# Kernel optimization log

Measured on AMD Instinct MI355X. Metric: run time of the kernel, lower is better.

The kernel has to match this reference:

```python
import jax, jax.numpy as jnp
import numpy as np

GRID_H, GRID_W, INPUT_DIM = 256, 256, 64
BATCH = 4096


def setup_inputs() -> dict:
    key = jax.random.key(0)
    k_in, k_w = jax.random.split(key)
    inputs = jax.random.uniform(k_in, (BATCH, INPUT_DIM), dtype=jnp.float32)
    # SOM weights initialized uniform[0,1) as in the original layer
    weights_map = jax.random.uniform(k_w, (GRID_H, GRID_W, INPUT_DIM), dtype=jnp.float32)
    return {"inputs": inputs, "weights_map": weights_map}


def reference(inputs, weights_map):
    """Inference forward of SOM2dLayer: find BMU coords + quantization error.

    inputs:      [B, D]
    weights_map: [H, W, D]
    returns (bmu_indices [B,2] int32, quantization_errors [B] float32)
    """
    H, W, D = weights_map.shape
    flat_w = weights_map.reshape(H * W, D)            # [N, D]
    x2 = jnp.sum(inputs * inputs, axis=1, keepdims=True)      # [B, 1]
    w2 = jnp.sum(flat_w * flat_w, axis=1)                     # [N]
    d2 = x2 - 2.0 * (inputs @ flat_w.T) + w2                  # [B, N]
    d2 = jnp.maximum(d2, 0.0)                                 # numerical floor
    bmu_flat = jnp.argmin(d2, axis=1)                         # [B]
    bmu_y = (bmu_flat // W).astype(jnp.int32)
    bmu_x = (bmu_flat % W).astype(jnp.int32)
    bmu_indices = jnp.stack([bmu_y, bmu_x], axis=1)           # [B, 2]
    min_d2 = jnp.take_along_axis(d2, bmu_flat[:, None], axis=1)[:, 0]
    quantization_errors = jnp.sqrt(min_d2)                    # [B]
    return bmu_indices, quantization_errors
```

## Files before the change

kernel.cpp:

```cpp
#include <hip/hip_runtime.h>
#include <math.h>


typedef short  bf16x8 __attribute__((ext_vector_type(8)));
typedef float  f32x4  __attribute__((ext_vector_type(4)));
typedef unsigned short u16;

constexpr int D     = 64;
constexpr int NW    = 65536;
constexpr int B     = 4096;
constexpr int NSUB  = 256;
constexpr int NFINE = NW / 16;
constexpr float MARG_HALF = 0.15f;

constexpr int STRIPS   = 32;
constexpr int STRIP_N  = NW / STRIPS;
constexpr int PANELS   = 8;
constexpr int ROWS_BLK = 128;

__device__ inline u16 bf16u(float f) {
    union { float f; unsigned u; } v; v.f = f;
    unsigned b = v.u;
    b += 0x7fffu + ((b >> 16) & 1u);
    return (u16)(b >> 16);
}

__device__ inline u16 bf16up(float f) {
    union { float f; unsigned u; } v; v.f = f;
    unsigned h = v.u >> 16;
    if ((v.u & 0xFFFFu) && !(v.u >> 31)) h += 1;
    return (u16)h;
}

__device__ __forceinline__ void gload_lds16(const void* g, void* l) {
    __builtin_amdgcn_global_load_lds(
        (const __attribute__((address_space(1))) unsigned int*)g,
        (__attribute__((address_space(3))) unsigned int*)l, 16, 0, 0);
}

__global__ __launch_bounds__(256) void k_prep(const float* __restrict__ w,
                                              const float* __restrict__ x,
                                              u16* __restrict__ whi,
                                              u16* __restrict__ xhi,
                                              float* __restrict__ w2c) {
    const int idx = blockIdx.x * 256 + threadIdx.x;
    if (idx < NW) {
        const float4* wr = reinterpret_cast<const float4*>(w + (size_t)idx * D);
        u16* orow = whi + (size_t)idx * D;
        float a0 = 0.f, a1 = 0.f, a2 = 0.f, a3 = 0.f;
#pragma unroll
        for (int h = 0; h < 8; ++h) {
            float4 v0 = wr[2 * h], v1 = wr[2 * h + 1];
            a0 = fmaf(v0.x, v0.x, a0); a1 = fmaf(v0.y, v0.y, a1);
            a2 = fmaf(v0.z, v0.z, a2); a3 = fmaf(v0.w, v0.w, a3);
            a0 = fmaf(v1.x, v1.x, a0); a1 = fmaf(v1.y, v1.y, a1);
            a2 = fmaf(v1.z, v1.z, a2); a3 = fmaf(v1.w, v1.w, a3);
            bf16x8 o = {(short)bf16u(v0.x), (short)bf16u(v0.y),
                        (short)bf16u(v0.z), (short)bf16u(v0.w),
                        (short)bf16u(v1.x), (short)bf16u(v1.y),
                        (short)bf16u(v1.z), (short)bf16u(v1.w)};
            *reinterpret_cast<bf16x8*>(orow + 8 * h) = o;
        }
        w2c[idx] = -0.5f * ((a0 + a1) + (a2 + a3));
    } else {
        const int r = idx - NW;
        const float4* xr = reinterpret_cast<const float4*>(x + (size_t)r * D);
        u16* orow = xhi + (size_t)r * D;
#pragma unroll
        for (int h = 0; h < 8; ++h) {
            float4 v0 = xr[2 * h], v1 = xr[2 * h + 1];
            bf16x8 o = {(short)bf16u(v0.x), (short)bf16u(v0.y),
                        (short)bf16u(v0.z), (short)bf16u(v0.w),
                        (short)bf16u(v1.x), (short)bf16u(v1.y),
                        (short)bf16u(v1.z), (short)bf16u(v1.w)};
            *reinterpret_cast<bf16x8*>(orow + 8 * h) = o;
        }
    }
}

template <int WRITE_FINE>
__global__ __launch_bounds__(256, 2) void k_screen0(
        const u16* __restrict__ whi, const u16* __restrict__ xhi,
        const float* __restrict__ w2c, float* __restrict__ pm,
        u16* __restrict__ pmf) {
    __shared__ __align__(16) char smem[32768];
    __shared__ __align__(16) float pmsh[512];
    const int bid   = blockIdx.x;
    const int strip = bid & 31;
    const int rbk   = bid >> 5;
    const int tid   = threadIdx.x;
    const int wv    = tid >> 6;
    const int lane  = tid & 63;
    const int col   = lane & 15;
    const int kg    = lane >> 4;
    const int row0  = rbk * ROWS_BLK;

    bf16x8 a[8][2];
#pragma unroll
    for (int rg = 0; rg < 8; ++rg)
#pragma unroll
        for (int h = 0; h < 2; ++h)
            a[rg][h] = *reinterpret_cast<const bf16x8*>(
                xhi + (size_t)(row0 + rg * 16 + col) * D + h * 32 + kg * 8);

    const char* wbase = (const char*)whi + (size_t)strip * STRIP_N * 128;
    unsigned soff[8];
#pragma unroll
    for (int i = 0; i < 8; ++i) {
        unsigned o = (unsigned)(i * 256 + tid) * 16;
        soff[i] = o ^ (((o >> 7) & 7u) << 4);
    }

    const unsigned msk = (unsigned)(col & 7) << 4;
    const float* w2s = w2c + strip * STRIP_N;

    float mx[8][4];
#pragma unroll
    for (int rg = 0; rg < 8; ++rg)
#pragma unroll
        for (int r = 0; r < 4; ++r) mx[rg][r] = -3.4e38f;

    for (int p = 0; p < PANELS; ++p) {
#pragma unroll
        for (int i = 0; i < 8; ++i)
            gload_lds16(wbase + (size_t)p * 32768 + soff[i],
                        &smem[i * 4096 + wv * 1024]);
        __syncthreads();

        const float* w2p = w2s + p * 256;
#pragma unroll
        for (int t = 0; t < 4; ++t) {
            const int nloc = wv * 64 + t * 16 + col;
            const unsigned u0 = (unsigned)nloc * 128 + kg * 16;
            const bf16x8 b0 = *reinterpret_cast<const bf16x8*>(smem + (u0 ^ msk));
            const bf16x8 b1 = *reinterpret_cast<const bf16x8*>(smem + ((u0 + 64) ^ msk));
            const float c = w2p[nloc];
            const f32x4 cq = {c, c, c, c};
#pragma unroll
            for (int rg = 0; rg < 8; ++rg) {
                f32x4 acc = __builtin_amdgcn_mfma_f32_16x16x32_bf16(a[rg][0], b0, cq, 0, 0, 0);
                acc = __builtin_amdgcn_mfma_f32_16x16x32_bf16(a[rg][1], b1, acc, 0, 0, 0);
                mx[rg][0] = fmaxf(mx[rg][0], acc[0]);
                mx[rg][1] = fmaxf(mx[rg][1], acc[1]);
                mx[rg][2] = fmaxf(mx[rg][2], acc[2]);
                mx[rg][3] = fmaxf(mx[rg][3], acc[3]);
            }
        }

        if ((p & 3) == 3) {
            const int s0 = strip * 8 + (p >> 2) * 4;
            const int s  = s0 + wv;

            __syncthreads();

            if (WRITE_FINE) {
                u16* st = reinterpret_cast<u16*>(smem);
#pragma unroll
                for (int rg = 0; rg < 8; ++rg)
#pragma unroll
                    for (int r = 0; r < 4; ++r)
                        st[wv * 2048 + (rg * 16 + kg * 4 + r) * 16 + col] =
                            bf16up(mx[rg][r]);
            }

#pragma unroll
            for (int rg = 0; rg < 8; ++rg) {
                float v0 = mx[rg][0], v1 = mx[rg][1], v2 = mx[rg][2], v3 = mx[rg][3];
#pragma unroll
                for (int sh = 1; sh < 16; sh <<= 1) {
                    v0 = fmaxf(v0, __shfl_xor(v0, sh, 64));
                    v1 = fmaxf(v1, __shfl_xor(v1, sh, 64));
                    v2 = fmaxf(v2, __shfl_xor(v2, sh, 64));
                    v3 = fmaxf(v3, __shfl_xor(v3, sh, 64));
                }
                float vv = v0;
                vv = (col == 1) ? v1 : vv;
                vv = (col == 2) ? v2 : vv;
                vv = (col == 3) ? v3 : vv;
                if (col < 4)
                    pmsh[(rg * 16 + kg * 4 + col) * 4 + wv] = vv;
                mx[rg][0] = -3.4e38f; mx[rg][1] = -3.4e38f;
                mx[rg][2] = -3.4e38f; mx[rg][3] = -3.4e38f;
            }

            __syncthreads();

            if (WRITE_FINE) {
                const char* src = smem + wv * 4096;
                char* dstg = (char*)pmf + ((size_t)s * 32 + rbk) * 4096;
#pragma unroll
                for (int i = 0; i < 4; ++i)
                    *reinterpret_cast<float4*>(dstg + i * 1024 + lane * 16) =
                        *reinterpret_cast<const float4*>(src + i * 1024 + lane * 16);
            }
            if (tid < 128) {
                float4 v = *reinterpret_cast<const float4*>(&pmsh[tid * 4]);
                *reinterpret_cast<float4*>(&pm[(size_t)(row0 + tid) * NSUB + s0]) = v;
            }
        }
        __syncthreads();
    }
}

template <int FINE>
__global__ __launch_bounds__(256) void k_rescore(
        const float* __restrict__ x, const float* __restrict__ w,
        const float* __restrict__ w2c, const float* __restrict__ pm,
        const u16* __restrict__ pmf, float* __restrict__ out) {
    const int wv   = threadIdx.x >> 6;
    const int lane = threadIdx.x & 63;
    const int row  = blockIdx.x * 4 + wv;
    const int rbk2 = row >> 7;
    const int rl   = row & 127;

    float pv[4];
#pragma unroll
    for (int it = 0; it < 4; ++it)
        pv[it] = pm[(size_t)row * NSUB + it * 64 + lane];
    float gm = fmaxf(fmaxf(pv[0], pv[1]), fmaxf(pv[2], pv[3]));
#pragma unroll
    for (int s = 1; s < 64; s <<= 1) gm = fmaxf(gm, __shfl_xor(gm, s, 64));
    const float thr = gm - MARG_HALF;

    const float4* xr = reinterpret_cast<const float4*>(x + (size_t)row * D);
    float4 xq[16];
#pragma unroll
    for (int q = 0; q < 16; ++q) xq[q] = xr[q];

    float bestv = 3.4e38f;
    int   besti = 0x7fffffff;

#pragma unroll
    for (int it = 0; it < 4; ++it) {
        unsigned long long bm = __ballot(pv[it] >= thr);
        while (bm) {
            int sb = __ffsll(bm) - 1;
            bm &= bm - 1;
            int sub  = it * 64 + sb;
            int base = (sub >> 3) * 2048 + ((sub >> 2) & 1) * 1024 + (sub & 3) * 64;

            if (FINE) {
                float fv = -3.4e38f;
                if (lane < 16) {
                    union { unsigned u; float f; } c;
                    c.u = (unsigned)pmf[((size_t)sub * 32 + rbk2) * 2048
                                        + rl * 16 + lane] << 16;
                    fv = c.f;
                }
                unsigned long long fm = __ballot(fv >= thr);
                while (fm) {
                    int colq = __ffsll(fm) - 1;
                    fm &= fm - 1;
                    int j = lane & 15, q = lane >> 4;
                    int n = base + (j >> 2) * 256 + (j & 3) * 16 + colq;
                    const float4* wr = reinterpret_cast<const float4*>(w + (size_t)n * D);
                    float d0 = 0.f, d1 = 0.f, d2 = 0.f, d3 = 0.f;
#pragma unroll
                    for (int k = 0; k < 4; ++k) {
                        float4 wq = wr[q * 4 + k];
                        float4 xv = xq[q * 4 + k];
                        d0 = fmaf(xv.x, wq.x, d0); d1 = fmaf(xv.y, wq.y, d1);
                        d2 = fmaf(xv.z, wq.z, d2); d3 = fmaf(xv.w, wq.w, d3);
                    }
                    float d = (d0 + d1) + (d2 + d3);
                    d += __shfl_xor(d, 16, 64);
                    d += __shfl_xor(d, 32, 64);
                    float val = -2.f * (d + w2c[n]);
                    if (val < bestv || (val == bestv && n < besti)) { bestv = val; besti = n; }
                }
            } else {
#pragma unroll
                for (int p4 = 0; p4 < 4; ++p4) {
                    int n = base + p4 * 256 + lane;
                    const float4* wr = reinterpret_cast<const float4*>(w + (size_t)n * D);
                    float d0 = 0.f, d1 = 0.f, d2 = 0.f, d3 = 0.f;
#pragma unroll
                    for (int q = 0; q < 16; ++q) {
                        float4 wq = wr[q];
                        d0 = fmaf(xq[q].x, wq.x, d0);
                        d1 = fmaf(xq[q].y, wq.y, d1);
                        d2 = fmaf(xq[q].z, wq.z, d2);
                        d3 = fmaf(xq[q].w, wq.w, d3);
                    }
                    float dot = (d0 + d1) + (d2 + d3);
                    float val = -2.f * (dot + w2c[n]);
                    if (val < bestv || (val == bestv && n < besti)) { bestv = val; besti = n; }
                }
            }
        }
    }
#pragma unroll
    for (int s = 1; s < 64; s <<= 1) {
        float ov = __shfl_xor(bestv, s, 64);
        int   oi = __shfl_xor(besti, s, 64);
        if (ov < bestv || (ov == bestv && oi < besti)) { bestv = ov; besti = oi; }
    }
    if (lane == 0) {
        float a0 = 0.f, a1 = 0.f, a2 = 0.f, a3 = 0.f;
#pragma unroll
        for (int q = 0; q < 16; ++q) {
            a0 = fmaf(xq[q].x, xq[q].x, a0);
            a1 = fmaf(xq[q].y, xq[q].y, a1);
            a2 = fmaf(xq[q].z, xq[q].z, a2);
            a3 = fmaf(xq[q].w, xq[q].w, a3);
        }
        float x2 = (a0 + a1) + (a2 + a3);
        float d2f = x2 + bestv;
        if (d2f < 0.f) d2f = 0.f;
        out[row * 2 + 0] = (float)(besti >> 8);
        out[row * 2 + 1] = (float)(besti & 255);
        out[2 * B + row] = sqrtf(d2f);
    }
}

__global__ __launch_bounds__(256) void fb_w2(const float* __restrict__ w,
                                             float* __restrict__ w2) {
    int n = blockIdx.x * 256 + threadIdx.x;
    const float4* wr = reinterpret_cast<const float4*>(w + (size_t)n * D);
    float a0 = 0.f, a1 = 0.f, a2 = 0.f, a3 = 0.f;
#pragma unroll
    for (int q = 0; q < 16; ++q) {
        float4 v = wr[q];
        a0 = fmaf(v.x, v.x, a0); a1 = fmaf(v.y, v.y, a1);
        a2 = fmaf(v.z, v.z, a2); a3 = fmaf(v.w, v.w, a3);
    }
    w2[n] = (a0 + a1) + (a2 + a3);
}

__global__ __launch_bounds__(256) void fb_main(const float* __restrict__ x,
                                               const float* __restrict__ w,
                                               const float* __restrict__ w2,
                                               float* __restrict__ ps,
                                               int* __restrict__ pi) {
    constexpr int NSTRIP = NW / 32;
    const int rb    = blockIdx.x & 15;
    const int strip = blockIdx.x >> 4;
    const int row   = rb * 256 + threadIdx.x;
    float xr[D];
    const float4* xrow = reinterpret_cast<const float4*>(x + (size_t)row * D);
#pragma unroll
    for (int q = 0; q < 16; ++q) {
        float4 v = xrow[q];
        xr[q * 4 + 0] = v.x; xr[q * 4 + 1] = v.y;
        xr[q * 4 + 2] = v.z; xr[q * 4 + 3] = v.w;
    }
    float best = 3.4e38f; int bidx = 0;
    const int n0 = strip * NSTRIP, n1 = n0 + NSTRIP;
    for (int n = n0; n < n1; ++n) {
        const float* wr = w + (size_t)n * D;
        float a0 = 0.f, a1 = 0.f, a2 = 0.f, a3 = 0.f;
#pragma unroll
        for (int d = 0; d < D; d += 4) {
            a0 = fmaf(xr[d + 0], wr[d + 0], a0);
            a1 = fmaf(xr[d + 1], wr[d + 1], a1);
            a2 = fmaf(xr[d + 2], wr[d + 2], a2);
            a3 = fmaf(xr[d + 3], wr[d + 3], a3);
        }
        float s = fmaf(-2.f, (a0 + a1) + (a2 + a3), w2[n]);
        if (s < best) { best = s; bidx = n; }
    }
    ps[(size_t)strip * B + row] = best;
    pi[(size_t)strip * B + row] = bidx;
}

__global__ __launch_bounds__(256) void fb_merge(const float* __restrict__ x,
                                                const float* __restrict__ ps,
                                                const int* __restrict__ pi,
                                                float* __restrict__ out) {
    int row = blockIdx.x * 256 + threadIdx.x;
    float bs = 3.5e38f; int bi = 0;
    for (int t = 0; t < 32; ++t) {
        float s = ps[(size_t)t * B + row];
        int   i = pi[(size_t)t * B + row];
        if (s < bs || (s == bs && i < bi)) { bs = s; bi = i; }
    }
    const float4* xrow = reinterpret_cast<const float4*>(x + (size_t)row * D);
    float a0 = 0.f, a1 = 0.f, a2 = 0.f, a3 = 0.f;
#pragma unroll
    for (int q = 0; q < 16; ++q) {
        float4 v = xrow[q];
        a0 = fmaf(v.x, v.x, a0); a1 = fmaf(v.y, v.y, a1);
        a2 = fmaf(v.z, v.z, a2); a3 = fmaf(v.w, v.w, a3);
    }
    float x2 = (a0 + a1) + (a2 + a3);
    float d2 = x2 + bs;
    if (d2 < 0.f) d2 = 0.f;
    out[row * 2 + 0] = (float)(bi >> 8);
    out[row * 2 + 1] = (float)(bi & 255);
    out[2 * B + row] = sqrtf(d2);
}

extern "C" void kernel_launch(void* const* d_in, const int* in_sizes, int n_in,
                              void* d_out, int out_size, void* d_ws, size_t ws_size,
                              hipStream_t stream) {
    const float* x = (const float*)d_in[0];
    const float* w = (const float*)d_in[1];
    float* out = (float*)d_out;

    const size_t whi_sz = (size_t)NW * D * 2;
    const size_t xhi_sz = (size_t)B * D * 2;
    const size_t w2c_sz = (size_t)NW * 4;
    const size_t pm_sz  = (size_t)B * NSUB * 4;
    const size_t pmf_sz = (size_t)NFINE * B * 2;
    const size_t need_c = whi_sz + xhi_sz + w2c_sz + pm_sz;
    const size_t need_f = need_c + pmf_sz;

    if (ws_size >= need_c) {
        char* p = (char*)d_ws;
        u16*   whi = (u16*)p;   p += whi_sz;
        u16*   xhi = (u16*)p;   p += xhi_sz;
        float* w2c = (float*)p; p += w2c_sz;
        float* pm  = (float*)p; p += pm_sz;
        u16*   pmf = (u16*)p;

        k_prep<<<(NW + B) / 256, 256, 0, stream>>>(w, x, whi, xhi, w2c);
        if (ws_size >= need_f) {
            k_screen0<1><<<STRIPS * (B / ROWS_BLK), 256, 0, stream>>>(whi, xhi, w2c, pm, pmf);
            k_rescore<1><<<B / 4, 256, 0, stream>>>(x, w, w2c, pm, pmf, out);
        } else {
            k_screen0<0><<<STRIPS * (B / ROWS_BLK), 256, 0, stream>>>(whi, xhi, w2c, pm, pmf);
            k_rescore<0><<<B / 4, 256, 0, stream>>>(x, w, w2c, pm, pmf, out);
        }
    } else {
        float* w2 = (float*)d_ws;
        float* ps = w2 + NW;
        int*   pi = (int*)(ps + (size_t)32 * B);
        fb_w2<<<NW / 256, 256, 0, stream>>>(w, w2);
        fb_main<<<16 * 32, 256, 0, stream>>>(x, w, w2, ps, pi);
        fb_merge<<<B / 256, 256, 0, stream>>>(x, ps, pi, out);
    }
}
```

Baseline: 113.4 us.

## Load screen weights directly from global per wave, dropping LDS staging

The screening kernel no longer stages weight panels into LDS with global_load_lds. Each wave now reads its own contiguous slice of bf16 weights straight from global memory into MFMA operands, which removes most block-level barriers. Because each wave now covers a contiguous range, the subgroup-to-column mapping changes, and the rescore kernel's base and index formulas are updated to match. The risk is that global-load latency is no longer hidden by LDS staging, and every row block re-reads the weights from cache.

```diff
diff --git a/kernel.cpp b/kernel.cpp
--- a/kernel.cpp
+++ b/kernel.cpp
@@ -15,8 +15,8 @@
 
 constexpr int STRIPS   = 32;
 constexpr int STRIP_N  = NW / STRIPS;
-constexpr int PANELS   = 8;
 constexpr int ROWS_BLK = 128;
+constexpr int WAVE_N   = STRIP_N / 4;
 
 __device__ inline u16 bf16u(float f) {
     union { float f; unsigned u; } v; v.f = f;
@@ -30,12 +30,6 @@
     unsigned h = v.u >> 16;
     if ((v.u & 0xFFFFu) && !(v.u >> 31)) h += 1;
     return (u16)h;
-}
-
-__device__ __forceinline__ void gload_lds16(const void* g, void* l) {
-    __builtin_amdgcn_global_load_lds(
-        (const __attribute__((address_space(1))) unsigned int*)g,
-        (__attribute__((address_space(3))) unsigned int*)l, 16, 0, 0);
 }
 
 __global__ __launch_bounds__(256) void k_prep(const float* __restrict__ w,
@@ -83,7 +77,7 @@
         const u16* __restrict__ whi, const u16* __restrict__ xhi,
         const float* __restrict__ w2c, float* __restrict__ pm,
         u16* __restrict__ pmf) {
-    __shared__ __align__(16) char smem[32768];
+    __shared__ __align__(16) u16 fsh[4][2048];
     __shared__ __align__(16) float pmsh[512];
     const int bid   = blockIdx.x;
     const int strip = bid & 31;
@@ -94,6 +88,7 @@
     const int col   = lane & 15;
     const int kg    = lane >> 4;
     const int row0  = rbk * ROWS_BLK;
+    const int W0    = strip * STRIP_N + wv * WAVE_N;
 
     bf16x8 a[8][2];
 #pragma unroll
@@ -103,100 +98,80 @@
             a[rg][h] = *reinterpret_cast<const bf16x8*>(
                 xhi + (size_t)(row0 + rg * 16 + col) * D + h * 32 + kg * 8);
 
-    const char* wbase = (const char*)whi + (size_t)strip * STRIP_N * 128;
-    unsigned soff[8];
-#pragma unroll
-    for (int i = 0; i < 8; ++i) {
-        unsigned o = (unsigned)(i * 256 + tid) * 16;
-        soff[i] = o ^ (((o >> 7) & 7u) << 4);
-    }
-
-    const unsigned msk = (unsigned)(col & 7) << 4;
-    const float* w2s = w2c + strip * STRIP_N;
-
     float mx[8][4];
 #pragma unroll
     for (int rg = 0; rg < 8; ++rg)
 #pragma unroll
         for (int r = 0; r < 4; ++r) mx[rg][r] = -3.4e38f;
 
-    for (int p = 0; p < PANELS; ++p) {
-#pragma unroll
-        for (int i = 0; i < 8; ++i)
-            gload_lds16(wbase + (size_t)p * 32768 + soff[i],
-                        &smem[i * 4096 + wv * 1024]);
+    for (int ch = 0; ch < 2; ++ch) {
+        for (int mo = 0; mo < 8; ++mo) {
+#pragma unroll
+            for (int mi = 0; mi < 2; ++mi) {
+                const int m = ch * 16 + mo * 2 + mi;
+                const int n = W0 + m * 16 + col;
+                const u16* wp = whi + (size_t)n * D + kg * 8;
+                const bf16x8 b0 = *reinterpret_cast<const bf16x8*>(wp);
+                const bf16x8 b1 = *reinterpret_cast<const bf16x8*>(wp + 32);
+                const float c = w2c[n];
+                const f32x4 cq = {c, c, c, c};
+#pragma unroll
+                for (int rg = 0; rg < 8; ++rg) {
+                    f32x4 acc = __builtin_amdgcn_mfma_f32_16x16x32_bf16(a[rg][0], b0, cq, 0, 0, 0);
+                    acc = __builtin_amdgcn_mfma_f32_16x16x32_bf16(a[rg][1], b1, acc, 0, 0, 0);
+                    mx[rg][0] = fmaxf(mx[rg][0], acc[0]);
+                    mx[rg][1] = fmaxf(mx[rg][1], acc[1]);
+                    mx[rg][2] = fmaxf(mx[rg][2], acc[2]);
+                    mx[rg][3] = fmaxf(mx[rg][3], acc[3]);
+                }
+            }
+        }
+
+        const int s_st = strip * 8 + ch * 4 + wv;
+
+        if (WRITE_FINE) {
+            u16* st = &fsh[wv][0];
+#pragma unroll
+            for (int rg = 0; rg < 8; ++rg)
+#pragma unroll
+                for (int r = 0; r < 4; ++r)
+                    st[(rg * 16 + kg * 4 + r) * 16 + col] = bf16up(mx[rg][r]);
+        }
+
+#pragma unroll
+        for (int rg = 0; rg < 8; ++rg) {
+            float v0 = mx[rg][0], v1 = mx[rg][1], v2 = mx[rg][2], v3 = mx[rg][3];
+#pragma unroll
+            for (int sh = 1; sh < 16; sh <<= 1) {
+                v0 = fmaxf(v0, __shfl_xor(v0, sh, 64));
+                v1 = fmaxf(v1, __shfl_xor(v1, sh, 64));
+                v2 = fmaxf(v2, __shfl_xor(v2, sh, 64));
+                v3 = fmaxf(v3, __shfl_xor(v3, sh, 64));
+            }
+            float vv = v0;
+            vv = (col == 1) ? v1 : vv;
+            vv = (col == 2) ? v2 : vv;
+            vv = (col == 3) ? v3 : vv;
+            if (col < 4)
+                pmsh[(rg * 16 + kg * 4 + col) * 4 + wv] = vv;
+            mx[rg][0] = -3.4e38f; mx[rg][1] = -3.4e38f;
+            mx[rg][2] = -3.4e38f; mx[rg][3] = -3.4e38f;
+        }
+
+        if (WRITE_FINE) {
+            const char* src = reinterpret_cast<const char*>(&fsh[wv][0]);
+            char* dst = (char*)pmf + ((size_t)s_st * 32 + rbk) * 4096;
+#pragma unroll
+            for (int i = 0; i < 4; ++i)
+                *reinterpret_cast<float4*>(dst + i * 1024 + lane * 16) =
+                    *reinterpret_cast<const float4*>(src + i * 1024 + lane * 16);
+        }
+
         __syncthreads();
-
-        const float* w2p = w2s + p * 256;
-#pragma unroll
-        for (int t = 0; t < 4; ++t) {
-            const int nloc = wv * 64 + t * 16 + col;
-            const unsigned u0 = (unsigned)nloc * 128 + kg * 16;
-            const bf16x8 b0 = *reinterpret_cast<const bf16x8*>(smem + (u0 ^ msk));
-            const bf16x8 b1 = *reinterpret_cast<const bf16x8*>(smem + ((u0 + 64) ^ msk));
-            const float c = w2p[nloc];
-            const f32x4 cq = {c, c, c, c};
-#pragma unroll
-            for (int rg = 0; rg < 8; ++rg) {
-                f32x4 acc = __builtin_amdgcn_mfma_f32_16x16x32_bf16(a[rg][0], b0, cq, 0, 0, 0);
-                acc = __builtin_amdgcn_mfma_f32_16x16x32_bf16(a[rg][1], b1, acc, 0, 0, 0);
-                mx[rg][0] = fmaxf(mx[rg][0], acc[0]);
-                mx[rg][1] = fmaxf(mx[rg][1], acc[1]);
-                mx[rg][2] = fmaxf(mx[rg][2], acc[2]);
-                mx[rg][3] = fmaxf(mx[rg][3], acc[3]);
-            }
-        }
-
-        if ((p & 3) == 3) {
-            const int s0 = strip * 8 + (p >> 2) * 4;
-            const int s  = s0 + wv;
-
-            __syncthreads();
-
-            if (WRITE_FINE) {
-                u16* st = reinterpret_cast<u16*>(smem);
-#pragma unroll
-                for (int rg = 0; rg < 8; ++rg)
-#pragma unroll
-                    for (int r = 0; r < 4; ++r)
-                        st[wv * 2048 + (rg * 16 + kg * 4 + r) * 16 + col] =
-                            bf16up(mx[rg][r]);
-            }
-
-#pragma unroll
-            for (int rg = 0; rg < 8; ++rg) {
-                float v0 = mx[rg][0], v1 = mx[rg][1], v2 = mx[rg][2], v3 = mx[rg][3];
-#pragma unroll
-                for (int sh = 1; sh < 16; sh <<= 1) {
-                    v0 = fmaxf(v0, __shfl_xor(v0, sh, 64));
-                    v1 = fmaxf(v1, __shfl_xor(v1, sh, 64));
-                    v2 = fmaxf(v2, __shfl_xor(v2, sh, 64));
-                    v3 = fmaxf(v3, __shfl_xor(v3, sh, 64));
-                }
-                float vv = v0;
-                vv = (col == 1) ? v1 : vv;
-                vv = (col == 2) ? v2 : vv;
-                vv = (col == 3) ? v3 : vv;
-                if (col < 4)
-                    pmsh[(rg * 16 + kg * 4 + col) * 4 + wv] = vv;
-                mx[rg][0] = -3.4e38f; mx[rg][1] = -3.4e38f;
-                mx[rg][2] = -3.4e38f; mx[rg][3] = -3.4e38f;
-            }
-
-            __syncthreads();
-
-            if (WRITE_FINE) {
-                const char* src = smem + wv * 4096;
-                char* dstg = (char*)pmf + ((size_t)s * 32 + rbk) * 4096;
-#pragma unroll
-                for (int i = 0; i < 4; ++i)
-                    *reinterpret_cast<float4*>(dstg + i * 1024 + lane * 16) =
-                        *reinterpret_cast<const float4*>(src + i * 1024 + lane * 16);
-            }
-            if (tid < 128) {
-                float4 v = *reinterpret_cast<const float4*>(&pmsh[tid * 4]);
-                *reinterpret_cast<float4*>(&pm[(size_t)(row0 + tid) * NSUB + s0]) = v;
-            }
+        if (tid < 128) {
+            float4 v = *reinterpret_cast<const float4*>(&pmsh[tid * 4]);
+            *reinterpret_cast<float4*>(
+                &pm[(size_t)(row0 + tid) * NSUB + strip * 8 + ch * 4]) = v;
         }
         __syncthreads();
     }
@@ -237,7 +212,7 @@
             int sb = __ffsll(bm) - 1;
             bm &= bm - 1;
             int sub  = it * 64 + sb;
-            int base = (sub >> 3) * 2048 + ((sub >> 2) & 1) * 1024 + (sub & 3) * 64;
+            int base = (sub >> 3) * 2048 + (sub & 3) * 512 + ((sub >> 2) & 1) * 256;
 
             if (FINE) {
                 float fv = -3.4e38f;
@@ -252,7 +227,7 @@
                     int colq = __ffsll(fm) - 1;
                     fm &= fm - 1;
                     int j = lane & 15, q = lane >> 4;
-                    int n = base + (j >> 2) * 256 + (j & 3) * 16 + colq;
+                    int n = base + j * 16 + colq;
                     const float4* wr = reinterpret_cast<const float4*>(w + (size_t)n * D);
                     float d0 = 0.f, d1 = 0.f, d2 = 0.f, d3 = 0.f;
 #pragma unroll
@@ -271,7 +246,7 @@
             } else {
 #pragma unroll
                 for (int p4 = 0; p4 < 4; ++p4) {
-                    int n = base + p4 * 256 + lane;
+                    int n = base + p4 * 64 + lane;
                     const float4* wr = reinterpret_cast<const float4*>(w + (size_t)n * D);
                     float d0 = 0.f, d1 = 0.f, d2 = 0.f, d3 = 0.f;
 #pragma unroll
```

Measured after the change: 121.6 us. 1.07x slower.
